# Kernel optimization log

Measured on AMD Instinct MI355X. Metric: run time of the kernel, lower is better.

## Reference

```python
import jax, jax.numpy as jnp
import numpy as np
import math

B, S, D = 2, 2048, 1024
LKV, LQ = 512, 768
H, HD = 16, 64          # decop_rot_dim must equal head_dim (code reshapes rot proj to head_dim)
E, NS, K = 8, 2, 2      # routed experts, shared experts, top-k
EPS = 1e-6


def rmsnorm(x, w):
    xf = x.astype(jnp.float32)
    n = xf * jax.lax.rsqrt(jnp.mean(xf * xf, axis=-1, keepdims=True) + EPS)
    return w * n.astype(x.dtype)


def rope(x, cos, sin):
    # x: (B,S,H,HD); cos/sin: (S, HD//2). Pairs are consecutive elements (view_as_complex).
    xr = x.reshape(*x.shape[:-1], HD // 2, 2)
    x0, x1 = xr[..., 0], xr[..., 1]
    c = cos[None, :, None, :]
    s = sin[None, :, None, :]
    o0 = x0 * c - x1 * s
    o1 = x0 * s + x1 * c
    return jnp.stack([o0, o1], axis=-1).reshape(x.shape)


def _expert(x, W1, b1, W2, b2):
    # Expert: Linear -> ReLU -> Linear -> Dropout(0.5); dropout is identity at eval.
    return jax.nn.relu(x @ W1 + b1) @ W2 + b2


def setup_inputs() -> dict:
    key = jax.random.key(0)
    ks = jax.random.split(key, 20)
    g = lambda i, shape: jax.random.normal(ks[i], shape, jnp.float32) * 0.02
    inv_freq = 1.0 / (10000.0 ** (jnp.arange(0, HD, 2, dtype=jnp.float32) / HD))
    ang = jnp.arange(S, dtype=jnp.float32)[:, None] * inv_freq[None, :]  # (S, HD//2)
    return {
        'x': jax.random.normal(ks[0], (B, S, D), jnp.float32),
        'freqs_cos': jnp.cos(ang),
        'freqs_sin': jnp.sin(ang),
        'router_noise': jax.random.normal(ks[1], (B, S, E), jnp.float32),
        'rms1_w': jnp.ones((D,), jnp.float32),
        'rms2_w': jnp.ones((D,), jnp.float32),
        'w_lq': g(2, (D, LQ)), 'w_lkv': g(3, (D, LKV)),
        'w_q': g(4, (LQ, H * HD)), 'w_k': g(5, (LKV, H * HD)), 'w_v': g(6, (LKV, H * HD)),
        'w_qr': g(7, (LQ, H * HD)), 'b_qr': jnp.zeros((H * HD,), jnp.float32),
        'w_kr': g(8, (D, H * HD)), 'b_kr': jnp.zeros((H * HD,), jnp.float32),
        'w_o': g(9, (H * HD, D)), 'b_o': jnp.zeros((D,), jnp.float32),
        'w_route': g(10, (D, E)), 'b_route': jnp.zeros((E,), jnp.float32),
        'w_noise': g(11, (D, E)), 'b_noise': jnp.zeros((E,), jnp.float32),
        'rW1': g(12, (E, D, 4 * D)), 'rb1': jnp.zeros((E, 4 * D), jnp.float32),
        'rW2': g(13, (E, 4 * D, D)), 'rb2': jnp.zeros((E, D), jnp.float32),
        'sW1': g(14, (NS, D, 4 * D)), 'sb1': jnp.zeros((NS, 4 * D), jnp.float32),
        'sW2': g(15, (NS, 4 * D, D)), 'sb2': jnp.zeros((NS, D), jnp.float32),
    }


def _forward(x, freqs_cos, freqs_sin, router_noise, rms1_w, rms2_w,
             w_lq, w_lkv, w_q, w_k, w_v, w_qr, b_qr, w_kr, b_kr, w_o, b_o,
             w_route, b_route, w_noise, b_noise,
             rW1, rb1, rW2, rb2, sW1, sb1, sW2, sb2):
    Bq, Sq, Dq = x.shape
    # --- MLA attention branch ---
    h = rmsnorm(x, rms1_w)
    cq = h @ w_lq          # (B,S,LQ)
    ckv = h @ w_lkv        # (B,S,LKV)
    q = (cq @ w_q).reshape(Bq, Sq, H, HD)
    qr = rope((cq @ w_qr + b_qr).reshape(Bq, Sq, H, HD), freqs_cos, freqs_sin)
    k = (ckv @ w_k).reshape(Bq, Sq, H, HD)
    kr = rope((h @ w_kr + b_kr).reshape(Bq, Sq, H, HD), freqs_cos, freqs_sin)
    v = (ckv @ w_v).reshape(Bq, Sq, H, HD)
    qf = jnp.concatenate([q, qr], axis=-1)  # (B,S,H,2*HD)
    kf = jnp.concatenate([k, kr], axis=-1)
    scores = jnp.einsum('bqhd,bkhd->bhqk', qf, kf) / math.sqrt(HD)  # scale by sqrt(head_dim), as in source
    att = jax.nn.softmax(scores.astype(jnp.float32), axis=-1).astype(qf.dtype)
    attn_out = jnp.einsum('bhqk,bkhd->bqhd', att, v).reshape(Bq, Sq, H * HD)
    x = x + attn_out @ w_o + b_o
    # --- DeepSeek MoE branch ---
    h2 = rmsnorm(x, rms2_w)
    r_act = h2 @ w_route + b_route
    noisy = r_act + router_noise * jax.nn.softplus(h2 @ w_noise + b_noise)
    topv, idx = jax.lax.top_k(noisy, K)
    # softmax over -inf-filled sparse logits == softmax over top-k values scattered to idx
    wk = jax.nn.softmax(topv, axis=-1)  # (B,S,K)
    gate = jnp.einsum('btk,btke->bte', wk, jax.nn.one_hot(idx, E, dtype=h2.dtype))  # zeros off top-k
    f = jnp.zeros_like(h2)
    for i in range(E):  # fixed small expert loop; gate is exactly 0 for unrouted tokens
        f = f + gate[..., i:i + 1] * _expert(h2, rW1[i], rb1[i], rW2[i], rb2[i])
    for j in range(NS):
        f = f + _expert(h2, sW1[j], sb1[j], sW2[j], sb2[j])
    # DeepSeekMoE returns x_in + f_out where x_in = rmsnorm output; Block adds residual
    return x + h2 + f


def reference(x, freqs_cos, freqs_sin, router_noise, rms1_w, rms2_w,
              w_lq, w_lkv, w_q, w_k, w_v, w_qr, b_qr, w_kr, b_kr, w_o, b_o,
              w_route, b_route, w_noise, b_noise,
              rW1, rb1, rW2, rb2, sW1, sb1, sW2, sb2):
    return _forward(x, freqs_cos, freqs_sin, router_noise, rms1_w, rms2_w,
                    w_lq, w_lkv, w_q, w_k, w_v, w_qr, b_qr, w_kr, b_kr, w_o, b_o,
                    w_route, b_route, w_noise, b_noise,
                    rW1, rb1, rW2, rb2, sW1, sb1, sW2, sb2)
```

## Files before the change

### kernel.cpp

```cpp
#include <hip/hip_runtime.h>
#include <cstdint>

typedef unsigned short u16;
typedef unsigned int   u32;
typedef unsigned long long u64;
using short8 = __attribute__((ext_vector_type(8))) short;
using f32x4  = __attribute__((ext_vector_type(4))) float;

#define S_   2048
#define D_   1024
#define NTOK 4096

__device__ __forceinline__ u16 f2bf(float f){
  u32 u = __float_as_uint(f);
  u32 r = u + 0x7fffu + ((u >> 16) & 1u);
  return (u16)(r >> 16);
}
__device__ __forceinline__ float bf2f(u16 h){
  return __uint_as_float(((u32)h) << 16);
}
__device__ __forceinline__ void gld16(const void* g, void* l){
  __builtin_amdgcn_global_load_lds((__attribute__((address_space(1))) void*)(void*)g,
                                   (__attribute__((address_space(3))) void*)l, 16, 0, 0);
}

enum { F_OUTBF16=1, F_BIAS=2, F_RELU=4, F_RESID=8, F_GATEACC=16,
       F_GATHER=64, F_SCATTER=128, F_EXPB=512, F_SPLITK2=1024, F_BIASHI=2048 };

template<int FLAGS>
__global__ void __launch_bounds__(256, 4)
gemm_k(const u16* __restrict__ A, int lda, long sAz,
       const u16* __restrict__ Bt, int ldb, long sBz,
       void* __restrict__ out, int ldo, long sOz,
       float* __restrict__ out2,
       const float* __restrict__ bias,
       const float* __restrict__ resid,
       const float* __restrict__ gv,
       const int* __restrict__ idx,
       const int* __restrict__ slotb,
       const int* __restrict__ cntp, int ebase,
       int K, int ncols)
{
  constexpr int BM = 128, BK = 32;
  const int tid = threadIdx.x;
  const int w = tid >> 6, l = tid & 63;
  const int wr = w >> 1, wc = w & 1;

  const int gx = gridDim.x, gy = gridDim.y;
  const int nwg = gx*gy*gridDim.z;
  const int flat = (blockIdx.z*gy + blockIdx.y)*gx + blockIdx.x;
  const int q8 = nwg >> 3, r8 = nwg & 7, xcd = flat & 7, off8 = flat >> 3;
  const int swz = (xcd < r8) ? (xcd*(q8+1) + off8)
                             : (r8*(q8+1) + (xcd-r8)*q8 + off8);
  const int tn = swz % gx;
  const int rest = swz / gx;
  const int tm = rest % gy;
  const int z  = rest / gy;
  const int ncol0 = tn * 128;

  int kh = 0, ze = z;
  if constexpr (FLAGS & F_SPLITK2){ kh = z & 1; ze = z >> 1; }

  int cnt = 0x7fffffff; long ofs = 0;
  if constexpr (FLAGS & (F_GATHER|F_SCATTER)){
    const int e = ebase + ze;
    cnt = cntp[e]; ofs = (long)cntp[8+e];
    if (tm*BM >= cnt) return;
  }

  const u16 *Abase, *Btbase;
  if constexpr (FLAGS & F_GATHER){
    Abase  = A;
    Btbase = Bt + (long)ze*sBz + (long)ncol0*ldb;
  } else if constexpr (FLAGS & F_SCATTER){
    Abase  = A + ofs*lda + (long)tm*BM*lda + (long)kh*K;
    Btbase = Bt + (long)ze*sBz + (long)ncol0*ldb + (long)kh*K;
  } else {
    Abase  = A  + (long)ze*sAz + (long)tm*BM*lda + (long)kh*K;
    Btbase = Bt + (long)ze*sBz + (long)ncol0*ldb + (long)kh*K;
  }

  const int r0 = tid >> 2, seg = tid & 3;
  long aoff0, aoff1;
  if constexpr (FLAGS & F_GATHER){
    const int p0 = tm*BM + r0, p1 = p0 + 64;
    const int t0 = (p0 < cnt) ? idx[ofs + p0] : 0;
    const int t1 = (p1 < cnt) ? idx[ofs + p1] : 0;
    aoff0 = (long)t0*lda; aoff1 = (long)t1*lda;
  } else {
    aoff0 = (long)r0*lda; aoff1 = (long)(r0+64)*lda;
  }
  const u16* pA0 = Abase + aoff0 + seg*8;
  const u16* pA1 = Abase + aoff1 + seg*8;
  const u16* pB0 = Btbase + (long)r0*ldb + seg*8;
  const u16* pB1 = Btbase + (long)(r0+64)*ldb + seg*8;

  __shared__ __align__(16) u16 As[2][BM*BK];
  __shared__ __align__(16) u16 Bs[2][BM*BK];

  f32x4 zero = {0.f,0.f,0.f,0.f};
  f32x4 acc[4][4];
  #pragma unroll
  for (int i=0;i<4;i++)
    #pragma unroll
    for (int j=0;j<4;j++) acc[i][j] = zero;

  const int NK = K >> 5;

  auto stage = [&](int buf, int kt){
    const int k0 = kt*BK;
    gld16(pA0 + k0, &As[buf][(w*64)*8]);
    gld16(pA1 + k0, &As[buf][(256 + w*64)*8]);
    gld16(pB0 + k0, &Bs[buf][(w*64)*8]);
    gld16(pB1 + k0, &Bs[buf][(256 + w*64)*8]);
  };

  stage(0,0);
  __syncthreads();

  for (int kt=0; kt<NK; ++kt){
    const int cur = kt & 1, nxt = cur ^ 1;
    if (kt+1 < NK) stage(nxt, kt+1);
    short8 a[4], b[4];
    #pragma unroll
    for (int m=0;m<4;m++){
      const int arow = wr*64 + m*16 + (l & 15);
      a[m] = *(const short8*)&As[cur][arow*BK + (l>>4)*8];
    }
    #pragma unroll
    for (int n=0;n<4;n++){
      const int brow = wc*64 + n*16 + (l & 15);
      b[n] = *(const short8*)&Bs[cur][brow*BK + (l>>4)*8];
    }
    #pragma unroll
    for (int m=0;m<4;m++)
      #pragma unroll
      for (int n=0;n<4;n++)
        acc[m][n] = __builtin_amdgcn_mfma_f32_16x16x32_bf16(a[m], b[n], acc[m][n], 0, 0, 0);
    __syncthreads();
  }

  float* outf = (float*)out + (long)z*sOz;
  u16*   outh = (u16*)out + (long)z*sOz;
  const float* bp = bias;
  if constexpr (FLAGS & F_EXPB) bp += (long)(ebase+ze)*ncols;
  const long row0 = (long)tm*BM + wr*64;
  #pragma unroll
  for (int m=0;m<4;m++){
    #pragma unroll
    for (int n=0;n<4;n++){
      const int col = ncol0 + wc*64 + n*16 + (l & 15);
      if (col < ncols){
        #pragma unroll
        for (int r=0;r<4;r++){
          const long row = row0 + m*16 + ((l>>4)*4) + r;
          float v = acc[m][n][r];
          if constexpr (FLAGS & F_BIAS){
            bool addb = true;
            if constexpr (FLAGS & F_SPLITK2) addb = (kh == 0);
            if (addb) v += bp[col];
          }
          if constexpr (FLAGS & F_BIASHI){
            if (col >= 1024) v += bias[col - 1024];
          }
          if constexpr (FLAGS & F_RELU) v = fmaxf(v, 0.f);
          if constexpr (FLAGS & F_SCATTER){
            if (row < cnt){
              const long gs = ofs + row;
              const int tok = idx[gs];
              float* dst = (float*)out + (long)(slotb[gs]*2 + kh)*sOz;
              dst[(long)tok*ldo + col] = gv[gs] * v;
            }
          } else if constexpr (FLAGS & F_GATHER){
            if (row < cnt) outh[(ofs + row)*(long)ldo + col] = f2bf(v);
          } else if constexpr (FLAGS & F_GATEACC){
            outf[row*(long)ldo + col] += v;
          } else if constexpr (FLAGS & F_RESID){
            const long off = row*(long)ldo + col;
            outf[off] = resid[off] + v;
          } else if constexpr (FLAGS & F_OUTBF16){
            outh[row*(long)ldo + col] = f2bf(v);
          } else {
            outf[row*(long)ldo + col] = v;
          }
        }
      }
    }
  }
}

#define LDP 136

__global__ void __launch_bounds__(256, 2)
flash_k(const u16* __restrict__ qf, const u16* __restrict__ kf,
        const u16* __restrict__ vt, u16* __restrict__ attn)
{
  const int bh = blockIdx.x;
  const int qt = blockIdx.y;
  const int b = bh >> 4, h = bh & 15;
  const int tid = threadIdx.x, w = tid >> 6, l = tid & 63;
  const int l4 = l & 15, lh = l >> 4;

  const u16* Qb = qf + (long)b*4194304 + h*128;
  const u16* Kb = kf + (long)b*4194304 + h*128;
  const u16* Vb = vt + (long)bh*131072;
  u16* Ob = attn + (long)b*2097152 + h*64;

  short8 qa[2][4];
  #pragma unroll
  for (int m=0;m<2;m++)
    #pragma unroll
    for (int ks=0;ks<4;ks++){
      const long row = qt*128 + w*32 + m*16 + l4;
      qa[m][ks] = *(const short8*)(Qb + row*2048 + ks*32 + lh*8);
    }

  __shared__ __align__(16) u16 KPs[128*LDP];
  __shared__ __align__(16) u16 Vs[64*LDP];

  const float SCL = 0.125f * 1.44269504f;
  float mst[2][4], lst[2][4];
  f32x4 o_acc[2][4];
  #pragma unroll
  for (int m=0;m<2;m++)
    #pragma unroll
    for (int r=0;r<4;r++){ mst[m][r] = -3.0e38f; lst[m][r] = 0.f; }
  #pragma unroll
  for (int m=0;m<2;m++)
    #pragma unroll
    for (int n=0;n<4;n++) o_acc[m][n] = (f32x4){0.f,0.f,0.f,0.f};

  for (int t=0;t<16;t++){
    #pragma unroll
    for (int i=0;i<8;i++){
      const int c = i*256 + tid;
      const int kr = c >> 4, kc = (c & 15) * 8;
      const uint4 v = *(const uint4*)(Kb + (long)(t*128+kr)*2048 + kc);
      *(uint4*)&KPs[kr*LDP + kc] = v;
    }
    #pragma unroll
    for (int i=0;i<4;i++){
      const int c = i*256 + tid;
      const int vr = c >> 4, vc = (c & 15) * 8;
      const uint4 v = *(const uint4*)(Vb + (long)vr*2048 + t*128 + vc);
      *(uint4*)&Vs[vr*LDP + vc] = v;
    }
    __syncthreads();

    f32x4 s[2][8];
    #pragma unroll
    for (int m=0;m<2;m++)
      #pragma unroll
      for (int n=0;n<8;n++) s[m][n] = (f32x4){0.f,0.f,0.f,0.f};
    #pragma unroll
    for (int ks=0;ks<4;ks++){
      short8 bn[8];
      #pragma unroll
      for (int n=0;n<8;n++)
        bn[n] = *(const short8*)&KPs[(n*16+l4)*LDP + ks*32 + lh*8];
      #pragma unroll
      for (int m=0;m<2;m++)
        #pragma unroll
        for (int n=0;n<8;n++)
          s[m][n] = __builtin_amdgcn_mfma_f32_16x16x32_bf16(qa[m][ks], bn[n], s[m][n], 0,0,0);
    }
    __syncthreads();

    #pragma unroll
    for (int m=0;m<2;m++){
      #pragma unroll
      for (int r=0;r<4;r++){
        float pm = s[m][0][r];
        #pragma unroll
        for (int n=1;n<8;n++) pm = fmaxf(pm, s[m][n][r]);
        #pragma unroll
        for (int o=1;o<16;o<<=1) pm = fmaxf(pm, __shfl_xor(pm, o));
        const float mnew = fmaxf(mst[m][r], pm);
        const float sf = exp2f((mst[m][r] - mnew)*SCL);
        float rsum = 0.f;
        #pragma unroll
        for (int n=0;n<8;n++){
          const float p = exp2f((s[m][n][r] - mnew)*SCL);
          s[m][n][r] = p;
          rsum += p;
        }
        #pragma unroll
        for (int o=1;o<16;o<<=1) rsum += __shfl_xor(rsum, o);
        lst[m][r] = lst[m][r]*sf + rsum;
        mst[m][r] = mnew;
        #pragma unroll
        for (int n=0;n<4;n++) o_acc[m][n][r] *= sf;
      }
    }
    #pragma unroll
    for (int m=0;m<2;m++)
      #pragma unroll
      for (int n=0;n<8;n++)
        #pragma unroll
        for (int r=0;r<4;r++)
          KPs[(w*32 + m*16 + lh*4 + r)*LDP + n*16 + l4] = f2bf(s[m][n][r]);
    __syncthreads();

    #pragma unroll
    for (int ks=0;ks<4;ks++){
      short8 pa[2], vb[4];
      #pragma unroll
      for (int m=0;m<2;m++)
        pa[m] = *(const short8*)&KPs[(w*32 + m*16 + l4)*LDP + ks*32 + lh*8];
      #pragma unroll
      for (int n=0;n<4;n++)
        vb[n] = *(const short8*)&Vs[(n*16+l4)*LDP + ks*32 + lh*8];
      #pragma unroll
      for (int m=0;m<2;m++)
        #pragma unroll
        for (int n=0;n<4;n++)
          o_acc[m][n] = __builtin_amdgcn_mfma_f32_16x16x32_bf16(pa[m], vb[n], o_acc[m][n], 0,0,0);
    }
    __syncthreads();
  }

  #pragma unroll
  for (int m=0;m<2;m++){
    #pragma unroll
    for (int r=0;r<4;r++){
      const long row = qt*128 + w*32 + m*16 + lh*4 + r;
      const float inv = 1.f / lst[m][r];
      #pragma unroll
      for (int n=0;n<4;n++)
        Ob[row*1024 + n*16 + l4] = f2bf(o_acc[m][n][r] * inv);
    }
  }
}

__global__ void tpose_k(const float* __restrict__ src, u16* __restrict__ dst,
                        int K, int N, long szS, long szD)
{
  __shared__ u16 tile[32][36];
  const int t = threadIdx.x;
  src += (long)blockIdx.z*szS; dst += (long)blockIdx.z*szD;
  const int n0 = blockIdx.x*32, k0 = blockIdx.y*32;
  const int lr = t >> 3, lc = (t & 7) * 4;
  const float4 v = *(const float4*)&src[(long)(k0+lr)*N + n0 + lc];
  ushort4 tv; tv.x=f2bf(v.x); tv.y=f2bf(v.y); tv.z=f2bf(v.z); tv.w=f2bf(v.w);
  *(ushort4*)&tile[lr][lc] = tv;
  __syncthreads();
  ushort4 o;
  o.x = tile[lc+0][lr]; o.y = tile[lc+1][lr];
  o.z = tile[lc+2][lr]; o.w = tile[lc+3][lr];
  *(ushort4*)&dst[(long)(n0+lr)*K + k0 + lc] = o;
}

__global__ void vt_k(const u16* __restrict__ kv, u16* __restrict__ dst)
{
  __shared__ u16 tile[32][36];
  const int t = threadIdx.x;
  const int z = blockIdx.z;
  const int b = z >> 4, h = z & 15;
  const int s0 = blockIdx.x*32, d0 = blockIdx.y*32;
  const int lr = t >> 3, lc = (t & 7) * 4;
  ushort4 v = *(const ushort4*)&kv[(long)(b*2048 + s0+lr)*2048 + 1024 + h*64 + d0 + lc];
  *(ushort4*)&tile[lr][lc] = v;
  __syncthreads();
  ushort4 o;
  o.x = tile[lc+0][lr]; o.y = tile[lc+1][lr];
  o.z = tile[lc+2][lr]; o.w = tile[lc+3][lr];
  *(ushort4*)&dst[(long)z*131072 + (long)(d0+lr)*2048 + s0 + lc] = o;
}

template<bool WF32>
__global__ void rmsnorm_k(const float* __restrict__ x, const float* __restrict__ w,
                          u16* __restrict__ ob, float* __restrict__ of)
{
  const int row = blockIdx.x, t = threadIdx.x;
  const float4 v = ((const float4*)(x + (long)row*D_))[t];
  float ss = v.x*v.x + v.y*v.y + v.z*v.z + v.w*v.w;
  #pragma unroll
  for (int o=32;o>0;o>>=1) ss += __shfl_down(ss, o);
  __shared__ float red[4];
  if ((t&63)==0) red[t>>6] = ss;
  __syncthreads();
  const float scale = rsqrtf((red[0]+red[1]+red[2]+red[3])*(1.0f/D_) + 1e-6f);
  const float4 wv = ((const float4*)w)[t];
  const float o0=v.x*scale*wv.x, o1=v.y*scale*wv.y, o2=v.z*scale*wv.z, o3=v.w*scale*wv.w;
  const long base = (long)row*D_ + t*4;
  uint2 p; p.x = (u32)f2bf(o0) | ((u32)f2bf(o1)<<16);
  p.y = (u32)f2bf(o2) | ((u32)f2bf(o3)<<16);
  *(uint2*)&ob[base] = p;
  if constexpr (WF32) *(float4*)&of[base] = make_float4(o0,o1,o2,o3);
}

__global__ void rope_concat_k(const u16* __restrict__ qqr, const u16* __restrict__ kv,
                              const u16* __restrict__ krt,
                              const float* __restrict__ fc, const float* __restrict__ fs,
                              u16* __restrict__ qf, u16* __restrict__ kf)
{
  const int idx = blockIdx.x*256 + threadIdx.x;
  const int j = idx & 31, h = (idx>>5) & 15, bs = idx >> 9;
  if (bs >= NTOK) return;
  const int s = bs & (S_-1);
  const float c = fc[s*32+j], sn = fs[s*32+j];
  const long ib2 = (long)bs*2048 + h*64 + 2*j;
  const long ib1 = (long)bs*1024 + h*64 + 2*j;
  const long ob = (long)bs*2048 + h*128 + 2*j;
  *(u32*)&qf[ob] = *(const u32*)&qqr[ib2];
  *(u32*)&kf[ob] = *(const u32*)&kv[ib2];
  float x0 = bf2f(qqr[ib2+1024]), x1 = bf2f(qqr[ib2+1025]);
  *(u32*)&qf[ob+64] = (u32)f2bf(x0*c - x1*sn) | ((u32)f2bf(x0*sn + x1*c) << 16);
  x0 = bf2f(krt[ib1]); x1 = bf2f(krt[ib1+1]);
  *(u32*)&kf[ob+64] = (u32)f2bf(x0*c - x1*sn) | ((u32)f2bf(x0*sn + x1*c) << 16);
}

__global__ void topk_k(const float* __restrict__ h2, const float* __restrict__ wr,
                       const float* __restrict__ br, const float* __restrict__ wn,
                       const float* __restrict__ bn, const float* __restrict__ noise,
                       int* __restrict__ eids, float2* __restrict__ gates)
{
  const int tok = blockIdx.x, t = threadIdx.x;
  const float4 xv = ((const float4*)(h2 + (long)tok*D_))[t];
  const float xs[4] = {xv.x, xv.y, xv.z, xv.w};
  float ar[8], an[8];
  #pragma unroll
  for (int e=0;e<8;e++){ ar[e]=0.f; an[e]=0.f; }
  #pragma unroll
  for (int i=0;i<4;i++){
    const int d = t*4+i;
    const float* wrr = wr + d*8;
    const float* wnr = wn + d*8;
    #pragma unroll
    for (int e=0;e<8;e++){ ar[e] += xs[i]*wrr[e]; an[e] += xs[i]*wnr[e]; }
  }
  #pragma unroll
  for (int e=0;e<8;e++){
    #pragma unroll
    for (int o=32;o>0;o>>=1){ ar[e] += __shfl_down(ar[e], o); an[e] += __shfl_down(an[e], o); }
  }
  __shared__ float rr[4][8], rn[4][8];
  if ((t&63)==0){
    const int w4 = t>>6;
    #pragma unroll
    for (int e=0;e<8;e++){ rr[w4][e]=ar[e]; rn[w4][e]=an[e]; }
  }
  __syncthreads();
  if (t==0){
    float nz[8];
    #pragma unroll
    for (int e=0;e<8;e++){
      const float r  = rr[0][e]+rr[1][e]+rr[2][e]+rr[3][e] + br[e];
      const float ns = rn[0][e]+rn[1][e]+rn[2][e]+rn[3][e] + bn[e];
      const float sp = (ns > 20.f) ? ns : log1pf(expf(ns));
      nz[e] = r + noise[(long)tok*8+e]*sp;
    }
    int i0 = 0;
    #pragma unroll
    for (int e=1;e<8;e++) if (nz[e] > nz[i0]) i0 = e;
    int i1 = -1; float best = -3.0e38f;
    #pragma unroll
    for (int e=0;e<8;e++) if (e != i0 && nz[e] > best){ best = nz[e]; i1 = e; }
    const float e1  = expf(nz[i1]-nz[i0]);
    const float inv = 1.f/(1.f+e1);
    eids[tok] = i0 | (i1 << 8);
    gates[tok] = make_float2(inv, e1*inv);
  }
}

__global__ void __launch_bounds__(64)
hist_k(const int* __restrict__ eids, int* __restrict__ segcnt)
{
  const int b = blockIdx.x, t = threadIdx.x;
  const int id = eids[b*64 + t];
  const int i0 = id & 255, i1 = (id >> 8) & 255;
  #pragma unroll
  for (int e=0;e<8;e++){
    const u64 m0 = __ballot(i0==e);
    const u64 m1 = __ballot(i1==e);
    if (t==0) segcnt[e*64+b] = __popcll(m0) + __popcll(m1);
  }
}

__global__ void __launch_bounds__(64)
scan_k(const int* __restrict__ segcnt, int* __restrict__ segoff,
       int* __restrict__ cntoff)
{
  const int t = threadIdx.x;
  int base = 0;
  for (int e=0;e<8;e++){
    const int c = segcnt[e*64+t];
    int sc = c;
    #pragma unroll
    for (int o=1;o<64;o<<=1){ int u = __shfl_up(sc, o); if (t >= o) sc += u; }
    const int tot = __shfl(sc, 63);
    segoff[e*64+t] = base + (sc - c);
    if (t==0){ cntoff[e] = tot; cntoff[8+e] = base; }
    base += tot;
  }
}

__global__ void __launch_bounds__(64)
fill_k(const int* __restrict__ eids, const float2* __restrict__ gates,
       const int* __restrict__ segoff, int* __restrict__ idxb,
       float* __restrict__ gvb, int* __restrict__ slotb)
{
  const int b = blockIdx.x, t = threadIdx.x;
  const int tok = b*64 + t;
  const int id = eids[tok];
  const int i0 = id & 255, i1 = (id >> 8) & 255;
  const float2 g = gates[tok];
  const u64 below = ((u64)1 << t) - 1;
  #pragma unroll
  for (int e=0;e<8;e++){
    const u64 m0 = __ballot(i0==e);
    const u64 m1 = __ballot(i1==e);
    if (i0==e){
      const int pos = segoff[e*64+b] + __popcll(m0 & below);
      idxb[pos] = tok; gvb[pos] = g.x; slotb[pos] = 0;
    } else if (i1==e){
      const int pos = segoff[e*64+b] + __popcll(m0) + __popcll(m1 & below);
      idxb[pos] = tok; gvb[pos] = g.y; slotb[pos] = 1;
    }
  }
}

__global__ void addstore_k(const float* __restrict__ a, const float* __restrict__ b,
                           float* __restrict__ o, long n4)
{
  long i = (long)blockIdx.x*blockDim.x + threadIdx.x;
  const long stride = (long)gridDim.x*blockDim.x;
  for (; i<n4; i+=stride){
    const float4 va = ((const float4*)a)[i];
    const float4 vb = ((const float4*)b)[i];
    ((float4*)o)[i] = make_float4(va.x+vb.x, va.y+vb.y, va.z+vb.z, va.w+vb.w);
  }
}
__global__ void addacc4_k(const float* __restrict__ f0, const float* __restrict__ f1,
                          const float* __restrict__ f2, const float* __restrict__ f3,
                          float* __restrict__ o, long n4)
{
  long i = (long)blockIdx.x*blockDim.x + threadIdx.x;
  const long stride = (long)gridDim.x*blockDim.x;
  for (; i<n4; i+=stride){
    const float4 a = ((const float4*)f0)[i];
    const float4 b = ((const float4*)f1)[i];
    const float4 c = ((const float4*)f2)[i];
    const float4 d = ((const float4*)f3)[i];
    float4 vo = ((const float4*)o)[i];
    ((float4*)o)[i] = make_float4(vo.x+a.x+b.x+c.x+d.x, vo.y+a.y+b.y+c.y+d.y,
                                  vo.z+a.z+b.z+c.z+d.z, vo.w+a.w+b.w+c.w+d.w);
  }
}

extern "C" void kernel_launch(void* const* d_in, const int* in_sizes, int n_in,
                              void* d_out, int out_size, void* d_ws, size_t ws_size,
                              hipStream_t stream)
{
  const float* x      = (const float*)d_in[0];
  const float* fcos   = (const float*)d_in[1];
  const float* fsin   = (const float*)d_in[2];
  const float* rnoise = (const float*)d_in[3];
  const float* rms1w  = (const float*)d_in[4];
  const float* rms2w  = (const float*)d_in[5];
  const float* w_lq   = (const float*)d_in[6];
  const float* w_lkv  = (const float*)d_in[7];
  const float* w_q    = (const float*)d_in[8];
  const float* w_k    = (const float*)d_in[9];
  const float* w_v    = (const float*)d_in[10];
  const float* w_qr   = (const float*)d_in[11];
  const float* b_qr   = (const float*)d_in[12];
  const float* w_kr   = (const float*)d_in[13];
  const float* b_kr   = (const float*)d_in[14];
  const float* w_o    = (const float*)d_in[15];
  const float* b_o    = (const float*)d_in[16];
  const float* w_route= (const float*)d_in[17];
  const float* b_route= (const float*)d_in[18];
  const float* w_noise= (const float*)d_in[19];
  const float* b_noise= (const float*)d_in[20];
  const float* rW1    = (const float*)d_in[21];
  const float* rb1    = (const float*)d_in[22];
  const float* rW2    = (const float*)d_in[23];
  const float* rb2    = (const float*)d_in[24];
  const float* sW1    = (const float*)d_in[25];
  const float* sb1    = (const float*)d_in[26];
  const float* sW2    = (const float*)d_in[27];
  const float* sb2    = (const float*)d_in[28];

  if (ws_size < 195166208ULL) return;

  char* ws = (char*)d_ws;
  u16*   h_bf    = (u16*)(ws + 0);
  u16*   cq_bf   = (u16*)(ws + 8388608);
  u16*   ckv_bf  = (u16*)(ws + 14680064);
  u16*   kr_tmp  = (u16*)(ws + 18874368);
  u16*   qf      = (u16*)(ws + 27262976);
  u16*   kf      = (u16*)(ws + 44040192);
  u16*   vt      = (u16*)(ws + 60817408);
  u16*   attn_bf = (u16*)(ws + 69468160);
  float* x1      = (float*)(ws + 77856768);
  float* h2f     = (float*)(ws + 94633984);
  u16*   h2_bf   = (u16*)(ws + 111411200);
  float* fb      = (float*)(ws + 119799808);
  u16*   Wt_g    = (u16*)(ws + 77856768);
  int*   cntoff  = (int*)(ws + 189005824);
  int*   eids    = (int*)(ws + 189006080);
  float2* gatesb = (float2*)(ws + 189022464);
  int*   idxb    = (int*)(ws + 189055232);
  float* gvb     = (float*)(ws + 189088000);
  int*   slotb   = (int*)(ws + 189120768);
  u16*   wo_t    = (u16*)(ws + 189153536);
  int*   segcnt  = (int*)(ws + 191250560);
  int*   segoff  = (int*)(ws + 191252608);
  u16*   qqr     = (u16*)(ws + 77856768);
  u16*   kv      = (u16*)(ws + 94633984);
  u16*   inter   = (u16*)(ws + 0);
  u16*   wlq_t   = (u16*)(ws + 119799808);
  u16*   wlkv_t  = (u16*)(ws + 121899008);
  u16*   wqqr_t  = (u16*)(ws + 123996160);
  u16*   wkv_t   = (u16*)(ws + 127141888);
  u16*   wkr_t   = (u16*)(ws + 129239040);

  const dim3 blk(256,1,1);
  #define GEMM(FL, GRID, ...) gemm_k<FL><<<GRID, blk, 0, stream>>>(__VA_ARGS__)
  #define NOSPARSE nullptr,nullptr,nullptr,nullptr,nullptr,nullptr,nullptr,0

  tpose_k<<<dim3(24,32),blk,0,stream>>>(w_lq,  wlq_t, 1024, 768, 0,0);
  tpose_k<<<dim3(16,32),blk,0,stream>>>(w_lkv, wlkv_t,1024, 512, 0,0);
  tpose_k<<<dim3(32,24),blk,0,stream>>>(w_q,   wqqr_t,            768,1024, 0,0);
  tpose_k<<<dim3(32,24),blk,0,stream>>>(w_qr,  wqqr_t + 1024*768, 768,1024, 0,0);
  tpose_k<<<dim3(32,16),blk,0,stream>>>(w_k,   wkv_t,             512,1024, 0,0);
  tpose_k<<<dim3(32,16),blk,0,stream>>>(w_v,   wkv_t + 1024*512,  512,1024, 0,0);
  tpose_k<<<dim3(32,32),blk,0,stream>>>(w_kr,  wkr_t, 1024,1024, 0,0);
  tpose_k<<<dim3(32,32),blk,0,stream>>>(w_o,   wo_t,  1024,1024, 0,0);

  rmsnorm_k<false><<<NTOK, blk, 0, stream>>>(x, rms1w, h_bf, nullptr);

  GEMM(F_OUTBF16, dim3(6,32,1),  h_bf,1024,0,  wlq_t,1024,0,  cq_bf,768,0,  NOSPARSE, 1024, 768);
  GEMM(F_OUTBF16, dim3(4,32,1),  h_bf,1024,0,  wlkv_t,1024,0, ckv_bf,512,0, NOSPARSE, 1024, 512);
  GEMM(F_OUTBF16|F_BIASHI, dim3(16,32,1), cq_bf,768,0,  wqqr_t,768,0, qqr,2048,0,
       nullptr, b_qr, nullptr,nullptr,nullptr,nullptr,nullptr,0, 768, 2048);
  GEMM(F_OUTBF16, dim3(16,32,1), ckv_bf,512,0, wkv_t,512,0,  kv,2048,0,  NOSPARSE, 512, 2048);
  GEMM(F_OUTBF16|F_BIAS, dim3(8,32,1), h_bf,1024,0, wkr_t,1024,0, kr_tmp,1024,0,
       nullptr, b_kr, nullptr,nullptr,nullptr,nullptr,nullptr,0, 1024, 1024);

  rope_concat_k<<<8192, blk, 0, stream>>>(qqr, kv, kr_tmp, fcos, fsin, qf, kf);
  vt_k<<<dim3(64,2,32), blk, 0, stream>>>(kv, vt);

  flash_k<<<dim3(32,16), blk, 0, stream>>>(qf, kf, vt, attn_bf);

  GEMM(F_BIAS|F_RESID, dim3(8,32,1), attn_bf,1024,0, wo_t,1024,0, x1,1024,0,
       nullptr, b_o, x, nullptr,nullptr,nullptr,nullptr,0, 1024, 1024);
  rmsnorm_k<true><<<NTOK, blk, 0, stream>>>(x1, rms2w, h2_bf, h2f);
  topk_k<<<NTOK, blk, 0, stream>>>(h2f, w_route, b_route, w_noise, b_noise, rnoise,
                                   eids, gatesb);
  hist_k<<<64, 64, 0, stream>>>(eids, segcnt);
  scan_k<<<1, 64, 0, stream>>>(segcnt, segoff, cntoff);
  fill_k<<<64, 64, 0, stream>>>(eids, gatesb, segoff, idxb, gvb, slotb);
  addstore_k<<<2048, blk, 0, stream>>>(x1, h2f, (float*)d_out, 1048576L);
  hipMemsetAsync(fb, 0, 67108864, stream);

  for (int g=0; g<2; ++g){
    const int eb = g*4;
    tpose_k<<<dim3(128,32,4),blk,0,stream>>>(rW1 + (long)eb*4194304, Wt_g, 1024, 4096,
                                             4194304L, 4194304L);
    GEMM(F_OUTBF16|F_BIAS|F_RELU|F_GATHER|F_EXPB, dim3(32,32,4),
         h2_bf,1024,0, Wt_g,1024,4194304L, inter,4096,0,
         nullptr, rb1, nullptr, nullptr, idxb, nullptr, cntoff, eb, 1024, 4096);
    tpose_k<<<dim3(32,128,4),blk,0,stream>>>(rW2 + (long)eb*4194304, Wt_g, 4096, 1024,
                                             4194304L, 4194304L);
    GEMM(F_BIAS|F_SCATTER|F_EXPB|F_SPLITK2, dim3(8,32,8),
         inter,4096,0, Wt_g,4096,4194304L, fb,1024,4194304L,
         nullptr, rb2, nullptr, gvb, idxb, slotb, cntoff, eb, 2048, 1024);
  }

  tpose_k<<<dim3(128,32,2),blk,0,stream>>>(sW1, Wt_g, 1024, 4096, 4194304L, 4194304L);
  GEMM(F_OUTBF16|F_BIAS|F_RELU, dim3(64,32,1), h2_bf,1024,0, Wt_g,1024,0, inter,8192,0,
       nullptr, sb1, nullptr,nullptr,nullptr,nullptr,nullptr,0, 1024, 8192);
  tpose_k<<<dim3(32,128,2),blk,0,stream>>>(sW2, Wt_g, 4096, 1024, 4194304L, 4194304L);
  GEMM(F_BIAS|F_GATEACC|F_EXPB|F_SPLITK2, dim3(8,32,4),
       inter,8192,4096, Wt_g,4096,4194304L, fb,1024,4194304L,
       nullptr, sb2, nullptr,nullptr,nullptr,nullptr,nullptr,0, 2048, 1024);

  addacc4_k<<<2048, blk, 0, stream>>>(fb, fb+4194304L, fb+8388608L, fb+12582912L,
                                      (float*)d_out, 1048576L);
}
```

Baseline: 1.110 ms.

## Split flash attention KV range across two blocks and merge partials

The flash attention kernel now splits the 16 KV tiles into two halves along a new grid z dimension. Each half writes unnormalized fp32 partial outputs plus row max and sum, and a new merge kernel rescales and combines them into bf16. This doubles the block count from 512 to 1024 to better fill the GPU's compute units, at the cost of extra fp32 global traffic and an additional kernel launch.

```diff
diff --git a/kernel.cpp b/kernel.cpp
--- a/kernel.cpp
+++ b/kernel.cpp
@@ -193,10 +193,12 @@
 
 __global__ void __launch_bounds__(256, 2)
 flash_k(const u16* __restrict__ qf, const u16* __restrict__ kf,
-        const u16* __restrict__ vt, u16* __restrict__ attn)
+        const u16* __restrict__ vt, float* __restrict__ opart,
+        float2* __restrict__ ml)
 {
   const int bh = blockIdx.x;
   const int qt = blockIdx.y;
+  const int kvh = blockIdx.z;
   const int b = bh >> 4, h = bh & 15;
   const int tid = threadIdx.x, w = tid >> 6, l = tid & 63;
   const int l4 = l & 15, lh = l >> 4;
@@ -204,7 +206,6 @@
   const u16* Qb = qf + (long)b*4194304 + h*128;
   const u16* Kb = kf + (long)b*4194304 + h*128;
   const u16* Vb = vt + (long)bh*131072;
-  u16* Ob = attn + (long)b*2097152 + h*64;
 
   short8 qa[2][4];
   #pragma unroll
@@ -230,7 +231,8 @@
     #pragma unroll
     for (int n=0;n<4;n++) o_acc[m][n] = (f32x4){0.f,0.f,0.f,0.f};
 
-  for (int t=0;t<16;t++){
+  const int t0 = kvh*8;
+  for (int t=t0; t<t0+8; t++){
     #pragma unroll
     for (int i=0;i<8;i++){
       const int c = i*256 + tid;
@@ -319,17 +321,43 @@
     __syncthreads();
   }
 
+  float* Op = opart + (long)kvh*4194304;
   #pragma unroll
   for (int m=0;m<2;m++){
     #pragma unroll
     for (int r=0;r<4;r++){
-      const long row = qt*128 + w*32 + m*16 + lh*4 + r;
-      const float inv = 1.f / lst[m][r];
+      const long srow = qt*128 + w*32 + m*16 + lh*4 + r;
+      const long obase = ((long)b*2048 + srow)*1024 + h*64;
       #pragma unroll
       for (int n=0;n<4;n++)
-        Ob[row*1024 + n*16 + l4] = f2bf(o_acc[m][n][r] * inv);
-    }
-  }
+        Op[obase + n*16 + l4] = o_acc[m][n][r];
+      if (l4 == 0)
+        ml[(long)kvh*65536 + (long)bh*2048 + srow] = make_float2(mst[m][r], lst[m][r]);
+    }
+  }
+}
+
+__global__ void pvmerge_k(const float* __restrict__ opart,
+                          const float2* __restrict__ ml,
+                          u16* __restrict__ attn)
+{
+  const int row = blockIdx.x;
+  const int t = threadIdx.x;
+  const int b = row >> 11, s = row & 2047;
+  const int h = t >> 4;
+  const float SCL = 0.125f * 1.44269504f;
+  const float2 m0 = ml[(long)(b*16+h)*2048 + s];
+  const float2 m1 = ml[65536L + (long)(b*16+h)*2048 + s];
+  const float mm = fmaxf(m0.x, m1.x);
+  const float s0 = exp2f((m0.x - mm)*SCL);
+  const float s1 = exp2f((m1.x - mm)*SCL);
+  const float inv = 1.f / (m0.y*s0 + m1.y*s1);
+  const float4 a = *(const float4*)&opart[(long)row*1024 + t*4];
+  const float4 c = *(const float4*)&opart[4194304L + (long)row*1024 + t*4];
+  uint2 pk;
+  pk.x = (u32)f2bf((a.x*s0 + c.x*s1)*inv) | ((u32)f2bf((a.y*s0 + c.y*s1)*inv) << 16);
+  pk.y = (u32)f2bf((a.z*s0 + c.z*s1)*inv) | ((u32)f2bf((a.w*s0 + c.w*s1)*inv) << 16);
+  *(uint2*)&attn[(long)row*1024 + t*4] = pk;
 }
 
 __global__ void tpose_k(const float* __restrict__ src, u16* __restrict__ dst,
@@ -610,6 +638,8 @@
   u16*   qqr     = (u16*)(ws + 77856768);
   u16*   kv      = (u16*)(ws + 94633984);
   u16*   inter   = (u16*)(ws + 0);
+  float* opart   = (float*)(ws + 77856768);
+  float2* mlbuf  = (float2*)(ws + 111411200);
   u16*   wlq_t   = (u16*)(ws + 119799808);
   u16*   wlkv_t  = (u16*)(ws + 121899008);
   u16*   wqqr_t  = (u16*)(ws + 123996160);
@@ -642,7 +672,8 @@
   rope_concat_k<<<8192, blk, 0, stream>>>(qqr, kv, kr_tmp, fcos, fsin, qf, kf);
   vt_k<<<dim3(64,2,32), blk, 0, stream>>>(kv, vt);
 
-  flash_k<<<dim3(32,16), blk, 0, stream>>>(qf, kf, vt, attn_bf);
+  flash_k<<<dim3(32,16,2), blk, 0, stream>>>(qf, kf, vt, opart, mlbuf);
+  pvmerge_k<<<NTOK, blk, 0, stream>>>(opart, mlbuf, attn_bf);
 
   GEMM(F_BIAS|F_RESID, dim3(8,32,1), attn_bf,1024,0, wo_t,1024,0, x1,1024,0,
        nullptr, b_o, x, nullptr,nullptr,nullptr,nullptr,0, 1024, 1024);
```

Result: no change. 1.093 ms (-1.5%).
